# Kernel optimization log

Measured on AMD Instinct MI355X. Metric: run time of the kernel, lower is better.

Reference implementation:

```python
import jax, jax.numpy as jnp
import numpy as np

R = 8            # ring rank
N = 4            # num cores
D_IN = 2048
D_OUT = 2048
LIN = [512, 512, 512, 512]   # local input dims (additive split)
LOUT = [512, 512, 512, 512]  # local output dims (additive split)


def setup_inputs() -> dict:
    key = jax.random.key(0)
    ks = jax.random.split(key, 6)
    inp = {"inputs": jax.random.normal(ks[0], (4, 1024, D_IN), dtype=jnp.float32)}
    for i in range(N):
        lf = LOUT[i] * LIN[i]
        std = np.sqrt(2.0 / (R + lf)).astype(np.float32)
        inp[f"core{i}"] = jax.random.normal(ks[1 + i], (R, lf, R), dtype=jnp.float32) * std
    inp["bias"] = jnp.zeros((D_OUT,), dtype=jnp.float32)
    return inp


def reference(inputs, core0, core1, core2, core3, bias):
    cores = [core0, core1, core2, core3]
    batch_shape = inputs.shape[:-1]
    x = inputs.reshape(-1, D_IN)                      # [B, D_IN]
    B = x.shape[0]

    # split input additively across cores
    offs = np.cumsum([0] + LIN)
    xs = [x[:, offs[i]:offs[i + 1]] for i in range(N)]  # each [B, d_in_i]
    Gs = [cores[i].reshape(R, LOUT[i], LIN[i], R) for i in range(N)]

    # environment messages: S_i[b,r,s] = sum_{o,x} G_i[r,o,x,s] * x_i[b,x]
    S = [jnp.einsum('roxs,bx->brs', Gs[i], xs[i]) for i in range(N)]

    eye = jnp.broadcast_to(jnp.eye(R, dtype=x.dtype), (B, R, R))
    # prefix P_i = S_0 ... S_{i-1}, suffix Q_i = S_{i+1} ... S_{N-1}
    P = [eye]
    for i in range(1, N):
        P.append(jnp.matmul(P[-1], S[i - 1]))
    Q = [eye]
    for i in range(N - 2, -1, -1):
        Q.append(jnp.matmul(S[i + 1], Q[-1]))
    Q = Q[::-1]

    outs = []
    for i in range(N):
        # Env_i[b,r,s] = sum_p Q_i[b,s,p] P_i[b,p,r]  (trace closure of the ring)
        env = jnp.einsum('bsp,bpr->brs', Q[i], P[i])
        # M_i[b,r,o,s] = sum_x G_i[r,o,x,s] x_i[b,x]
        M = jnp.einsum('roxs,bx->bros', Gs[i], xs[i])
        outs.append(jnp.einsum('brs,bros->bo', env, M))
    out = jnp.concatenate(outs, axis=-1) + bias       # [B, D_OUT]
    return out.reshape(batch_shape + (D_OUT,))
```

## Files before the change

kernel.cpp:

```cpp
#include <hip/hip_runtime.h>
#include <stdint.h>

#define B_TOT   4096
#define D_IN    2048
#define D_OUT   2048
#define NCHUNK  4
#define LIN     512
#define LOUT    512
#define RK      8
#define CORE_R_STRIDE 2097152
#define CORE_O_STRIDE 4096

#define WS_XT    0
#define WS_GHAT  8388608
#define WS_S     (8388608 + 131072)
#define WS_ENVT  (8388608 + 131072 + 1048576)

typedef __attribute__((ext_vector_type(8))) __bf16 bf16x8;
typedef __attribute__((ext_vector_type(4))) float f32x4;
typedef __attribute__((ext_vector_type(4))) unsigned int u32x4;

__global__ __launch_bounds__(256) void k_transpose(const float* __restrict__ x,
                                                   float* __restrict__ xT) {
    __shared__ float tile[32][33];
    int b0 = blockIdx.x * 32;
    int c0 = blockIdx.y * 32;
    int tx = threadIdx.x;
    int ty = threadIdx.y;
#pragma unroll
    for (int j = 0; j < 4; ++j)
        tile[ty + j * 8][tx] = x[(size_t)(b0 + ty + j * 8) * D_IN + c0 + tx];
    __syncthreads();
#pragma unroll
    for (int j = 0; j < 4; ++j)
        xT[(size_t)(c0 + ty + j * 8) * B_TOT + b0 + tx] = tile[tx][ty + j * 8];
}

__global__ __launch_bounds__(256) void k_reduce_g(const float* __restrict__ g0,
                                                  const float* __restrict__ g1,
                                                  const float* __restrict__ g2,
                                                  const float* __restrict__ g3,
                                                  float* __restrict__ ghat) {
    int i = blockIdx.z;
    int r = blockIdx.y;
    int xs = blockIdx.x * 256 + threadIdx.x;
    const float* G = (i == 0) ? g0 : (i == 1) ? g1 : (i == 2) ? g2 : g3;
    const float* base = G + (size_t)r * CORE_R_STRIDE + xs;
    float acc = 0.f;
#pragma unroll 8
    for (int o = 0; o < LOUT; ++o) acc += base[(size_t)o * CORE_O_STRIDE];
    ghat[(size_t)i * 32768 + r * 4096 + xs] = acc;
}

__global__ __launch_bounds__(256) void k_s(const float* __restrict__ x,
                                           const float* __restrict__ ghat,
                                           float* __restrict__ S) {
    int i = blockIdx.y;
    int tid = threadIdx.x;
    int rs = tid & 63;
    int b = blockIdx.x * 4 + (tid >> 6);
    int r = rs >> 3, s = rs & 7;
    const float* gh = ghat + (size_t)i * 32768 + r * 4096 + s;
    const float* xr = x + (size_t)b * D_IN + i * LIN;
    float acc = 0.f;
#pragma unroll 8
    for (int xi = 0; xi < LIN; ++xi) acc = fmaf(gh[xi * 8], xr[xi], acc);
    S[(size_t)i * (B_TOT * 64) + b * 64 + rs] = acc;
}

__device__ __forceinline__ float mm8(float A, float B, int lane) {
    float c = 0.f;
#pragma unroll
    for (int p = 0; p < 8; ++p) {
        float a = __shfl(A, (lane & 56) | p, 64);
        float b = __shfl(B, (p << 3) | (lane & 7), 64);
        c = fmaf(a, b, c);
    }
    return c;
}
__device__ __forceinline__ float tr8(float E, int lane) {
    return __shfl(E, ((lane & 7) << 3) | (lane >> 3), 64);
}

__global__ __launch_bounds__(256) void k_env(const float* __restrict__ S,
                                             float* __restrict__ envT) {
    int tid = threadIdx.x;
    int lane = tid & 63;
    int b = blockIdx.x * 4 + (tid >> 6);
    float S0 = S[0 * (B_TOT * 64) + b * 64 + lane];
    float S1 = S[1 * (B_TOT * 64) + b * 64 + lane];
    float S2 = S[2 * (B_TOT * 64) + b * 64 + lane];
    float S3 = S[3 * (B_TOT * 64) + b * 64 + lane];

    float P1 = S0;
    float P2 = mm8(P1, S1, lane);
    float P3 = mm8(P2, S2, lane);
    float Q2 = S3;
    float Q1 = mm8(S2, Q2, lane);
    float Q0 = mm8(S1, Q1, lane);

    float e0 = tr8(Q0, lane);
    float e1 = tr8(mm8(Q1, P1, lane), lane);
    float e2 = tr8(mm8(Q2, P2, lane), lane);
    float e3 = tr8(P3, lane);

    envT[(size_t)(0 * 64 + lane) * B_TOT + b] = e0;
    envT[(size_t)(1 * 64 + lane) * B_TOT + b] = e1;
    envT[(size_t)(2 * 64 + lane) * B_TOT + b] = e2;
    envT[(size_t)(3 * 64 + lane) * B_TOT + b] = e3;
}

__device__ __forceinline__ uint2 split2pk(float a, float b) {
    unsigned int h, l;
    asm("v_cvt_pk_bf16_f32 %0, %1, %2" : "=v"(h) : "v"(a), "v"(b));
    float fa = __uint_as_float(h << 16);
    float fb = __uint_as_float(h & 0xffff0000u);
    float la = a - fa;
    float lb = b - fb;
    asm("v_cvt_pk_bf16_f32 %0, %1, %2" : "=v"(l) : "v"(la), "v"(lb));
    return make_uint2(h, l);
}

__global__ __launch_bounds__(256, 2) void k_gemm_pipe2(const float* __restrict__ g0,
                                                       const float* __restrict__ g1,
                                                       const float* __restrict__ g2,
                                                       const float* __restrict__ g3,
                                                       const float* __restrict__ xT,
                                                       const float* __restrict__ envT,
                                                       const float* __restrict__ bias,
                                                       float* __restrict__ out) {
    int l = blockIdx.x;
    int c = (l & 7) | (((l >> 3) >> 5) << 3);
    int b_idx = (l >> 3) & 31;
    int i = c >> 2;
    int o0 = (c & 3) * 128;
    int b0 = b_idx * 128;

    const float* G = (i == 0) ? g0 : (i == 1) ? g1 : (i == 2) ? g2 : g3;
    const float* xTi = xT + (size_t)i * LIN * B_TOT;
    const float* eTi = envT + (size_t)i * 64 * B_TOT;

    __shared__ __align__(16) short Bhi[2][5120];
    __shared__ __align__(16) short Blo[2][5120];

    const int tid = threadIdx.x;
    const int lane = tid & 63;
    const int wave = tid >> 6;
    const int wm = (wave >> 1) * 64;
    const int wn = (wave & 1) * 64;
    const int l15 = lane & 15;
    const int quad = lane >> 4;

    const int so = tid >> 1;
    const int sh = (tid & 1) * 16;
    const int s0 = (tid & 1) * 2;
    const float* gsrc = G + (size_t)(o0 + so) * CORE_O_STRIDE + sh;

    f32x4 acc[4][4];
#pragma unroll
    for (int mf = 0; mf < 4; ++mf)
#pragma unroll
        for (int nf = 0; nf < 4; ++nf) acc[mf][nf] = (f32x4){0.f, 0.f, 0.f, 0.f};

    float4 fA0, fA1, fA2, fA3;
    float4 fB0, fB1, fB2, fB3;

    auto LOADGA = [&](int tn) {
        const float* p = gsrc + (size_t)(tn >> 7) * CORE_R_STRIDE + (tn & 127) * 32;
        fA0 = *(const float4*)(p);
        fA1 = *(const float4*)(p + 4);
        fA2 = *(const float4*)(p + 8);
        fA3 = *(const float4*)(p + 12);
    };
    auto LOADGB = [&](int tn) {
        const float* p = gsrc + (size_t)(tn >> 7) * CORE_R_STRIDE + (tn & 127) * 32;
        fB0 = *(const float4*)(p);
        fB1 = *(const float4*)(p + 4);
        fB2 = *(const float4*)(p + 8);
        fB3 = *(const float4*)(p + 12);
    };
    auto STOREA = [&](int pb) {
        u32x4 H0, L0, H1, L1;
        uint2 q;
        q = split2pk(fA0.x, fA0.y); H0.x = q.x; L0.x = q.y;
        q = split2pk(fA0.z, fA0.w); H0.y = q.x; L0.y = q.y;
        q = split2pk(fA1.x, fA1.y); H0.z = q.x; L0.z = q.y;
        q = split2pk(fA1.z, fA1.w); H0.w = q.x; L0.w = q.y;
        q = split2pk(fA2.x, fA2.y); H1.x = q.x; L1.x = q.y;
        q = split2pk(fA2.z, fA2.w); H1.y = q.x; L1.y = q.y;
        q = split2pk(fA3.x, fA3.y); H1.z = q.x; L1.z = q.y;
        q = split2pk(fA3.z, fA3.w); H1.w = q.x; L1.w = q.y;
        *(u32x4*)&Bhi[pb][(so * 5 + s0) * 8]     = H0;
        *(u32x4*)&Bhi[pb][(so * 5 + s0 + 1) * 8] = H1;
        *(u32x4*)&Blo[pb][(so * 5 + s0) * 8]     = L0;
        *(u32x4*)&Blo[pb][(so * 5 + s0 + 1) * 8] = L1;
    };
    auto STOREB = [&](int pb) {
        u32x4 H0, L0, H1, L1;
        uint2 q;
        q = split2pk(fB0.x, fB0.y); H0.x = q.x; L0.x = q.y;
        q = split2pk(fB0.z, fB0.w); H0.y = q.x; L0.y = q.y;
        q = split2pk(fB1.x, fB1.y); H0.z = q.x; L0.z = q.y;
        q = split2pk(fB1.z, fB1.w); H0.w = q.x; L0.w = q.y;
        q = split2pk(fB2.x, fB2.y); H1.x = q.x; L1.x = q.y;
        q = split2pk(fB2.z, fB2.w); H1.y = q.x; L1.y = q.y;
        q = split2pk(fB3.x, fB3.y); H1.z = q.x; L1.z = q.y;
        q = split2pk(fB3.z, fB3.w); H1.w = q.x; L1.w = q.y;
        *(u32x4*)&Bhi[pb][(so * 5 + s0) * 8]     = H0;
        *(u32x4*)&Bhi[pb][(so * 5 + s0 + 1) * 8] = H1;
        *(u32x4*)&Blo[pb][(so * 5 + s0) * 8]     = L0;
        *(u32x4*)&Blo[pb][(so * 5 + s0 + 1) * 8] = L1;
    };

    float xc[4];
#pragma unroll
    for (int mf = 0; mf < 4; ++mf)
        xc[mf] = xTi[(size_t)quad * B_TOT + b0 + wm + mf * 16 + l15];

    float e[4][8];

    auto COMP = [&](int p, int kk) {
        float xn[4];
#pragma unroll
        for (int mf = 0; mf < 4; ++mf)
            xn[mf] = xTi[(size_t)(((kk + 1) & 127) * 4 + quad) * B_TOT
                         + b0 + wm + mf * 16 + l15];

        bf16x8 bh[4], bl[4];
#pragma unroll
        for (int nf = 0; nf < 4; ++nf) {
            int n = wn + nf * 16 + l15;
            bh[nf] = *(const bf16x8*)&Bhi[p][(n * 5 + quad) * 8];
            bl[nf] = *(const bf16x8*)&Blo[p][(n * 5 + quad) * 8];
        }

        __builtin_amdgcn_s_setprio(1);
#pragma unroll
        for (int mf = 0; mf < 4; ++mf) {
            float xv = xc[mf];
            u32x4 AH, AL;
            uint2 pr;
            pr = split2pk(e[mf][0] * xv, e[mf][1] * xv); AH.x = pr.x; AL.x = pr.y;
            pr = split2pk(e[mf][2] * xv, e[mf][3] * xv); AH.y = pr.x; AL.y = pr.y;
            pr = split2pk(e[mf][4] * xv, e[mf][5] * xv); AH.z = pr.x; AL.z = pr.y;
            pr = split2pk(e[mf][6] * xv, e[mf][7] * xv); AH.w = pr.x; AL.w = pr.y;
            bf16x8 Ah = __builtin_bit_cast(bf16x8, AH);
            bf16x8 Al = __builtin_bit_cast(bf16x8, AL);
#pragma unroll
            for (int nf = 0; nf < 4; ++nf) {
                acc[mf][nf] = __builtin_amdgcn_mfma_f32_16x16x32_bf16(Ah, bh[nf], acc[mf][nf], 0, 0, 0);
                acc[mf][nf] = __builtin_amdgcn_mfma_f32_16x16x32_bf16(Ah, bl[nf], acc[mf][nf], 0, 0, 0);
                acc[mf][nf] = __builtin_amdgcn_mfma_f32_16x16x32_bf16(Al, bh[nf], acc[mf][nf], 0, 0, 0);
            }
        }
        __builtin_amdgcn_s_setprio(0);
#pragma unroll
        for (int mf = 0; mf < 4; ++mf) xc[mf] = xn[mf];
    };

    LOADGA(0);
    LOADGB(1);
    STOREA(0);
    __syncthreads();

    int t = 0;
    for (int r = 0; r < 8; ++r) {
#pragma unroll
        for (int mf = 0; mf < 4; ++mf) {
            int m = b0 + wm + mf * 16 + l15;
#pragma unroll
            for (int s = 0; s < 8; ++s)
                e[mf][s] = eTi[(size_t)(r * 8 + s) * B_TOT + m];
        }
        for (int kk = 0; kk < 128; kk += 2, t += 2) {
            if (t + 2 < 1024) LOADGA(t + 2);
            COMP(0, kk);
            STOREB(1);
            __syncthreads();
            if (t + 3 < 1024) LOADGB(t + 3);
            COMP(1, kk + 1);
            if (t + 2 < 1024) STOREA(0);
            __syncthreads();
        }
    }

#pragma unroll
    for (int nf = 0; nf < 4; ++nf) {
        int col = o0 + wn + nf * 16 + l15;
        float bv = bias[i * LOUT + col];
#pragma unroll
        for (int mf = 0; mf < 4; ++mf) {
#pragma unroll
            for (int reg = 0; reg < 4; ++reg) {
                int row = b0 + wm + mf * 16 + quad * 4 + reg;
                out[(size_t)row * D_OUT + i * LOUT + col] = acc[mf][nf][reg] + bv;
            }
        }
    }
}

extern "C" void kernel_launch(void* const* d_in, const int* in_sizes, int n_in,
                              void* d_out, int out_size, void* d_ws, size_t ws_size,
                              hipStream_t stream) {
    const float* x    = (const float*)d_in[0];
    const float* g0   = (const float*)d_in[1];
    const float* g1   = (const float*)d_in[2];
    const float* g2   = (const float*)d_in[3];
    const float* g3   = (const float*)d_in[4];
    const float* bias = (const float*)d_in[5];
    float* out = (float*)d_out;
    float* ws = (float*)d_ws;

    float* xT   = ws + WS_XT;
    float* ghat = ws + WS_GHAT;
    float* S    = ws + WS_S;
    float* envT = ws + WS_ENVT;

    k_transpose<<<dim3(128, 64), dim3(32, 8), 0, stream>>>(x, xT);
    k_reduce_g<<<dim3(16, 8, 4), 256, 0, stream>>>(g0, g1, g2, g3, ghat);
    k_s<<<dim3(1024, 4), 256, 0, stream>>>(x, ghat, S);
    k_env<<<1024, 256, 0, stream>>>(S, envT);
    k_gemm_pipe2<<<512, 256, 0, stream>>>(g0, g1, g2, g3, xT, envT, bias, out);
}
```

Baseline: 2.122 ms.

## Split GEMM rank loop across two workgroups and add partial-sum reduce kernel

The main GEMM kernel can now split its 8-step rank loop into two halves, launching twice as many workgroups. Each half writes a partial output into workspace, and a new elementwise kernel sums the two partials and adds the bias. The aim is more parallelism and better latency hiding across CUs. The cost is extra global traffic for the partial buffers plus an additional kernel launch. The block-to-XCD index mapping is also changed, and the split runs only when the workspace is large enough.

```diff
diff --git a/kernel.cpp b/kernel.cpp
--- a/kernel.cpp
+++ b/kernel.cpp
@@ -15,6 +15,9 @@
 #define WS_GHAT  8388608
 #define WS_S     (8388608 + 131072)
 #define WS_ENVT  (8388608 + 131072 + 1048576)
+#define WS_POUT  10616832
+#define OUT_ELEMS 8388608ull
+#define WS_SPLIT_NEED_BYTES 109576192ull
 
 typedef __attribute__((ext_vector_type(8))) __bf16 bf16x8;
 typedef __attribute__((ext_vector_type(4))) float f32x4;
@@ -128,13 +131,21 @@
                                                        const float* __restrict__ xT,
                                                        const float* __restrict__ envT,
                                                        const float* __restrict__ bias,
-                                                       float* __restrict__ out) {
+                                                       float* __restrict__ pout,
+                                                       int nsplit) {
     int l = blockIdx.x;
-    int c = (l & 7) | (((l >> 3) >> 5) << 3);
-    int b_idx = (l >> 3) & 31;
+    int per_xcd = (int)(gridDim.x >> 3);
+    int wgid = (l & 7) * per_xcd + (l >> 3);
+    int cr = wgid >> 5;
+    int b_idx = wgid & 31;
+    int c, rh, nr;
+    if (nsplit == 2) { c = cr >> 1; rh = cr & 1; nr = 4; }
+    else             { c = cr;      rh = 0;      nr = 8; }
+    int rstart = rh * 4;
     int i = c >> 2;
     int o0 = (c & 3) * 128;
     int b0 = b_idx * 128;
+    const int TMAX = nr * 128;
 
     const float* G = (i == 0) ? g0 : (i == 1) ? g1 : (i == 2) ? g2 : g3;
     const float* xTi = xT + (size_t)i * LIN * B_TOT;
@@ -154,7 +165,8 @@
     const int so = tid >> 1;
     const int sh = (tid & 1) * 16;
     const int s0 = (tid & 1) * 2;
-    const float* gsrc = G + (size_t)(o0 + so) * CORE_O_STRIDE + sh;
+    const float* gsrc = G + (size_t)rstart * CORE_R_STRIDE
+                          + (size_t)(o0 + so) * CORE_O_STRIDE + sh;
 
     f32x4 acc[4][4];
 #pragma unroll
@@ -264,39 +276,56 @@
     __syncthreads();
 
     int t = 0;
-    for (int r = 0; r < 8; ++r) {
+    for (int r = 0; r < nr; ++r) {
 #pragma unroll
         for (int mf = 0; mf < 4; ++mf) {
             int m = b0 + wm + mf * 16 + l15;
 #pragma unroll
             for (int s = 0; s < 8; ++s)
-                e[mf][s] = eTi[(size_t)(r * 8 + s) * B_TOT + m];
+                e[mf][s] = eTi[(size_t)((rstart + r) * 8 + s) * B_TOT + m];
         }
         for (int kk = 0; kk < 128; kk += 2, t += 2) {
-            if (t + 2 < 1024) LOADGA(t + 2);
+            if (t + 2 < TMAX) LOADGA(t + 2);
             COMP(0, kk);
             STOREB(1);
             __syncthreads();
-            if (t + 3 < 1024) LOADGB(t + 3);
+            if (t + 3 < TMAX) LOADGB(t + 3);
             COMP(1, kk + 1);
-            if (t + 2 < 1024) STOREA(0);
+            if (t + 2 < TMAX) STOREA(0);
             __syncthreads();
         }
     }
 
+    float* dst = pout + (size_t)rh * OUT_ELEMS;
+    const bool addb = (nsplit == 1);
 #pragma unroll
     for (int nf = 0; nf < 4; ++nf) {
         int col = o0 + wn + nf * 16 + l15;
-        float bv = bias[i * LOUT + col];
+        float bv = addb ? bias[i * LOUT + col] : 0.f;
 #pragma unroll
         for (int mf = 0; mf < 4; ++mf) {
 #pragma unroll
             for (int reg = 0; reg < 4; ++reg) {
                 int row = b0 + wm + mf * 16 + quad * 4 + reg;
-                out[(size_t)row * D_OUT + i * LOUT + col] = acc[mf][nf][reg] + bv;
+                dst[(size_t)row * D_OUT + i * LOUT + col] = acc[mf][nf][reg] + bv;
             }
         }
     }
+}
+
+__global__ __launch_bounds__(256) void k_reduce_out(const float* __restrict__ part,
+                                                    const float* __restrict__ bias,
+                                                    float* __restrict__ out) {
+    size_t idx = (size_t)blockIdx.x * 256 + threadIdx.x;
+    const float4 a = *(const float4*)(part + idx * 4);
+    const float4 b = *(const float4*)(part + OUT_ELEMS + idx * 4);
+    const float4 bv = *(const float4*)(bias + (idx & 511) * 4);
+    float4 o;
+    o.x = a.x + b.x + bv.x;
+    o.y = a.y + b.y + bv.y;
+    o.z = a.z + b.z + bv.z;
+    o.w = a.w + b.w + bv.w;
+    *(float4*)(out + idx * 4) = o;
 }
 
 extern "C" void kernel_launch(void* const* d_in, const int* in_sizes, int n_in,
@@ -315,10 +344,21 @@
     float* ghat = ws + WS_GHAT;
     float* S    = ws + WS_S;
     float* envT = ws + WS_ENVT;
+    float* pout = ws + WS_POUT;
+
+    int nsplit = (ws_size >= WS_SPLIT_NEED_BYTES) ? 2 : 1;
 
     k_transpose<<<dim3(128, 64), dim3(32, 8), 0, stream>>>(x, xT);
     k_reduce_g<<<dim3(16, 8, 4), 256, 0, stream>>>(g0, g1, g2, g3, ghat);
     k_s<<<dim3(1024, 4), 256, 0, stream>>>(x, ghat, S);
     k_env<<<1024, 256, 0, stream>>>(S, envT);
-    k_gemm_pipe2<<<512, 256, 0, stream>>>(g0, g1, g2, g3, xT, envT, bias, out);
-}
+
+    if (nsplit == 2) {
+        k_gemm_pipe2<<<1024, 256, 0, stream>>>(g0, g1, g2, g3, xT, envT, bias,
+                                               pout, 2);
+        k_reduce_out<<<8192, 256, 0, stream>>>(pout, bias, out);
+    } else {
+        k_gemm_pipe2<<<512, 256, 0, stream>>>(g0, g1, g2, g3, xT, envT, bias,
+                                              out, 1);
+    }
+}
```

Result: no change. 2.138 ms (+0.8%).
